# Kernel tuning notes

Hardware: AMD Instinct MI355X
Metric: run time of the kernel (lower is better)

The kernel has to match this reference:

```python
import jax, jax.numpy as jnp
import numpy as np

N, NB, EU, ED, EB = 40000, 60000, 200000, 200000, 120000
D, H = 256, 256
BN_EPS = 1e-5


def _bn(x, g, b):
    # training-mode BatchNorm1d over the cell dimension (biased variance)
    mu = jnp.mean(x, axis=0)
    var = jnp.mean((x - mu) ** 2, axis=0)
    return g * (x - mu) * jax.lax.rsqrt(var + BN_EPS) + b


def _mlp(x, W1, b1, g1, c1, W2, b2, g2, c2):
    # update nn: Linear -> BN -> ReLU -> Linear -> BN -> ReLU
    h = jax.nn.relu(_bn(x @ W1 + b1, g1, c1))
    return jax.nn.relu(_bn(h @ W2 + b2, g2, c2))


def _forward(x, up_attr, down_attr, boundary_attr, Wmu, bmu, Wmd, bmd,
             W1u, b1u, g1u, c1u, W2u, b2u, g2u, c2u,
             W1d, b1d, g1d, c1d, W2d, b2d, g2d, c2d,
             W1b, b1b, g1b, c1b, W2b, b2b, g2b, c2b,
             Wc, bc, gc, cc, eps1, eps2, eps3,
             up_index, down_index, boundary_index):
    n, d = x.shape
    # msg_up_nn = ReLU(Linear(cat[x_j, up_attr])); split W to avoid materializing cat
    mu = jax.nn.relu(x[up_index[0]] @ Wmu[:d] + up_attr @ Wmu[d:] + bmu)
    agg_up = jax.ops.segment_sum(mu, up_index[1], num_segments=n)
    md = jax.nn.relu(x[down_index[0]] @ Wmd[:d] + down_attr @ Wmd[d:] + bmd)
    agg_down = jax.ops.segment_sum(md, down_index[1], num_segments=n)
    # msg_boundaries_nn is identity: gather boundary cell features, sum to targets
    agg_bnd = jax.ops.segment_sum(boundary_attr[boundary_index[0]], boundary_index[1], num_segments=n)
    out_up = _mlp(agg_up + (1.0 + eps1) * x, W1u, b1u, g1u, c1u, W2u, b2u, g2u, c2u)
    out_down = _mlp(agg_down + (1.0 + eps2) * x, W1d, b1d, g1d, c1d, W2d, b2d, g2d, c2d)
    out_bnd = _mlp(agg_bnd + (1.0 + eps3) * x, W1b, b1b, g1b, c1b, W2b, b2b, g2b, c2b)
    comb = jnp.concatenate([out_up, out_down, out_bnd], axis=-1)
    return jax.nn.relu(_bn(comb @ Wc + bc, gc, cc))


def setup_inputs() -> dict:
    key = jax.random.key(0)
    ks = iter(jax.random.split(key, 64))

    def nrm(shape, scale=1.0):
        return jax.random.normal(next(ks), shape, dtype=jnp.float32) * scale

    inp = {}
    inp['x'] = nrm((N, D))
    inp['up_attr'] = nrm((EU, D))
    inp['down_attr'] = nrm((ED, D))
    inp['boundary_attr'] = nrm((NB, D))
    s_msg = 1.0 / np.sqrt(2 * D)
    inp['Wmu'] = nrm((2 * D, D), s_msg); inp['bmu'] = jnp.zeros((D,), jnp.float32)
    inp['Wmd'] = nrm((2 * D, D), s_msg); inp['bmd'] = jnp.zeros((D,), jnp.float32)
    s1, s2 = 1.0 / np.sqrt(D), 1.0 / np.sqrt(H)
    for t in ('u', 'd', 'b'):
        inp['W1' + t] = nrm((D, H), s1); inp['b1' + t] = jnp.zeros((H,), jnp.float32)
        inp['g1' + t] = jnp.ones((H,), jnp.float32); inp['c1' + t] = jnp.zeros((H,), jnp.float32)
        inp['W2' + t] = nrm((H, H), s2); inp['b2' + t] = jnp.zeros((H,), jnp.float32)
        inp['g2' + t] = jnp.ones((H,), jnp.float32); inp['c2' + t] = jnp.zeros((H,), jnp.float32)
    inp['Wc'] = nrm((3 * H, H), 1.0 / np.sqrt(3 * H)); inp['bc'] = jnp.zeros((H,), jnp.float32)
    inp['gc'] = jnp.ones((H,), jnp.float32); inp['cc'] = jnp.zeros((H,), jnp.float32)
    inp['eps1'] = jnp.zeros((1,), jnp.float32)
    inp['eps2'] = jnp.zeros((1,), jnp.float32)
    inp['eps3'] = jnp.zeros((1,), jnp.float32)
    inp['up_index'] = jax.random.randint(next(ks), (2, EU), 0, N)
    inp['down_index'] = jax.random.randint(next(ks), (2, ED), 0, N)
    bsrc = jax.random.randint(next(ks), (EB,), 0, NB)
    btgt = jax.random.randint(next(ks), (EB,), 0, N)
    inp['boundary_index'] = jnp.stack([bsrc, btgt], axis=0)
    return inp


def reference(x, up_attr, down_attr, boundary_attr, Wmu, bmu, Wmd, bmd,
              W1u, b1u, g1u, c1u, W2u, b2u, g2u, c2u,
              W1d, b1d, g1d, c1d, W2d, b2d, g2d, c2d,
              W1b, b1b, g1b, c1b, W2b, b2b, g2b, c2b,
              Wc, bc, gc, cc, eps1, eps2, eps3,
              up_index, down_index, boundary_index):
    return _forward(x, up_attr, down_attr, boundary_attr, Wmu, bmu, Wmd, bmd,
                    W1u, b1u, g1u, c1u, W2u, b2u, g2u, c2u,
                    W1d, b1d, g1d, c1d, W2d, b2d, g2d, c2d,
                    W1b, b1b, g1b, c1b, W2b, b2b, g2b, c2b,
                    Wc, bc, gc, cc, eps1, eps2, eps3,
                    up_index, down_index, boundary_index)
```

## Files before the change

kernel.cpp:

```cpp
#include <hip/hip_runtime.h>
#include <hip/hip_bf16.h>
#include <stdint.h>

#define NCELL 40000
#define EUE   200000
#define EDE   200000
#define EBE   120000
#define NM    ((size_t)NCELL * 256)

typedef __attribute__((ext_vector_type(8))) short bf16x8;
typedef __attribute__((ext_vector_type(4))) float f32x4;

__device__ __forceinline__ uint16_t f2bf(float f) {
  union { float f; uint32_t u; } v; v.f = f;
  uint32_t u = v.u;
  u += 0x7fffu + ((u >> 16) & 1u);
  return (uint16_t)(u >> 16);
}

struct WArgs {
  const float* src[11];
  uint16_t*    dst[11];
  int          K[11];
};

__global__ void k_wconv(WArgs a) {
  int m = blockIdx.z;
  int K = a.K[m];
  int k0 = blockIdx.x * 32;
  if (k0 >= K) return;
  int n0 = blockIdx.y * 32;
  __shared__ float t[32][33];
  int tx = threadIdx.x, ty = threadIdx.y;
  const float* src = a.src[m];
  for (int i = ty; i < 32; i += 8)
    t[i][tx] = src[(size_t)(k0 + i) * 256 + n0 + tx];
  __syncthreads();
  uint16_t* dst = a.dst[m];
  for (int i = ty; i < 32; i += 8)
    dst[(size_t)(n0 + i) * K + k0 + tx] = f2bf(t[tx][i]);
}

__global__ void k_count(const int* __restrict__ tgt, int* __restrict__ cnt, int E) {
  int i = blockIdx.x * 256 + threadIdx.x;
  if (i < E) atomicAdd(&cnt[tgt[i]], 1);
}

struct ScanArgs { const int* cnt[3]; int* offs[3]; int* head[3]; };

__global__ void k_scan(ScanArgs a) {
  int s = blockIdx.x;
  const int n = NCELL;
  const int* cnt = a.cnt[s];
  int* offs = a.offs[s];
  int* head = a.head[s];
  __shared__ int buf[1024];
  __shared__ int carry;
  int tid = threadIdx.x;
  if (tid == 0) carry = 0;
  __syncthreads();
  for (int base = 0; base < n; base += 1024) {
    int i = base + tid;
    int v = (i < n) ? cnt[i] : 0;
    buf[tid] = v;
    __syncthreads();
    for (int d = 1; d < 1024; d <<= 1) {
      int t = (tid >= d) ? buf[tid - d] : 0;
      __syncthreads();
      buf[tid] += t;
      __syncthreads();
    }
    int excl = carry + buf[tid] - v;
    if (i < n) { offs[i] = excl; head[i] = excl; }
    __syncthreads();
    if (tid == 1023) carry += buf[1023];
    __syncthreads();
  }
  if (tid == 0) offs[n] = carry;
}

__global__ void k_fill(const int* __restrict__ src, const int* __restrict__ tgt,
                       int* __restrict__ head, int* __restrict__ perm,
                       int* __restrict__ psrc, int E) {
  int e = blockIdx.x * 256 + threadIdx.x;
  if (e < E) {
    int p = atomicAdd(&head[tgt[e]], 1);
    perm[p] = e;
    psrc[p] = src[e];
  }
}

__global__ void k_segsum(const float* __restrict__ MSG, const int* __restrict__ offs,
                         const float* __restrict__ x, const float* __restrict__ eps,
                         float* __restrict__ out) {
  int t = blockIdx.x;
  int c = threadIdx.x * 4;
  int s = offs[t], e = offs[t + 1];
  float sE = 1.f + *eps;
  float4 xa = *(const float4*)(x + (size_t)t * 256 + c);
  float a0 = xa.x * sE, a1 = xa.y * sE, a2 = xa.z * sE, a3 = xa.w * sE;
  for (int j = s; j < e; j++) {
    float4 v = *(const float4*)(MSG + (size_t)j * 256 + c);
    a0 += v.x; a1 += v.y; a2 += v.z; a3 += v.w;
  }
  *(float4*)(out + (size_t)t * 256 + c) = make_float4(a0, a1, a2, a3);
}

__global__ void k_bgather(const float* __restrict__ battr, const int* __restrict__ offs,
                          const int* __restrict__ psrc, const float* __restrict__ x,
                          const float* __restrict__ eps, float* __restrict__ out) {
  int t = blockIdx.x;
  int c = threadIdx.x * 4;
  int s = offs[t], e = offs[t + 1];
  float sE = 1.f + *eps;
  float4 xa = *(const float4*)(x + (size_t)t * 256 + c);
  float a0 = xa.x * sE, a1 = xa.y * sE, a2 = xa.z * sE, a3 = xa.w * sE;
  for (int j = s; j < e; j++) {
    int sr = psrc[j];
    float4 v = *(const float4*)(battr + (size_t)sr * 256 + c);
    a0 += v.x; a1 += v.y; a2 += v.z; a3 += v.w;
  }
  *(float4*)(out + (size_t)t * 256 + c) = make_float4(a0, a1, a2, a3);
}

__global__ void k_bnrelu(const float* __restrict__ Y, const float* __restrict__ s12,
                         const float* __restrict__ g, const float* __restrict__ cb,
                         float* __restrict__ out, int ldo) {
  int i = blockIdx.x * 256 + threadIdx.x;
  int c = (i & 63) * 4;
  size_t row = (size_t)(i >> 6);
  const float invN = 1.f / (float)NCELL;
  float4 v = *(const float4*)(Y + row * 256 + c);
  float vv[4] = {v.x, v.y, v.z, v.w};
  float o[4];
#pragma unroll
  for (int k = 0; k < 4; k++) {
    float mean = s12[c + k] * invN;
    float var  = s12[256 + c + k] * invN - mean * mean;
    float sc = g[c + k] * rsqrtf(var + 1e-5f);
    float sh = cb[c + k] - mean * sc;
    o[k] = fmaxf(vv[k] * sc + sh, 0.f);
  }
  *(float4*)(out + row * (size_t)ldo + c) = make_float4(o[0], o[1], o[2], o[3]);
}

template <int MODE>
__global__ __launch_bounds__(256)
void k_gemm(const float* __restrict__ A, int lda, const uint16_t* __restrict__ Bt, int K,
            const float* __restrict__ bias, float* __restrict__ C, float* __restrict__ stats,
            const int* __restrict__ perm, const int* __restrict__ psrc,
            const float* __restrict__ XT, int M) {
  __shared__ uint16_t Al[128 * 32];
  __shared__ uint16_t Bl[128 * 32];
  const int tid = threadIdx.x;
  const int m0 = blockIdx.x * 128;
  const int n0 = blockIdx.y * 128;
  const int lane = tid & 63;
  const int wave = tid >> 6;
  const int wr = (wave >> 1) * 64;
  const int wc = (wave & 1) * 64;
  const int lm = lane & 15;
  const int lq = lane >> 4;

  f32x4 acc[4][4];
#pragma unroll
  for (int i = 0; i < 4; i++)
#pragma unroll
    for (int j = 0; j < 4; j++)
      acc[i][j] = f32x4{0.f, 0.f, 0.f, 0.f};

  const int arow = tid >> 3;
  const int acol = (tid & 7) * 4;

  int pidx[4];
#pragma unroll
  for (int rr = 0; rr < 4; rr++) {
    int gr = m0 + arow + rr * 32;
    if (MODE == 1) pidx[rr] = (gr < M) ? perm[gr] : -1;
    else           pidx[rr] = (gr < M) ? gr : -1;
  }

  for (int kt = 0; kt < K; kt += 32) {
#pragma unroll
    for (int rr = 0; rr < 4; rr++) {
      int r = arow + rr * 32;
      float4 v = make_float4(0.f, 0.f, 0.f, 0.f);
      if (pidx[rr] >= 0) v = *(const float4*)(A + (size_t)pidx[rr] * lda + kt + acol);
      union { uint16_t h[4]; uint2 u; } p;
      p.h[0] = f2bf(v.x); p.h[1] = f2bf(v.y); p.h[2] = f2bf(v.z); p.h[3] = f2bf(v.w);
      *(uint2*)(Al + r * 32 + acol) = p.u;
    }
#pragma unroll
    for (int ss = 0; ss < 2; ss++) {
      int j = tid + ss * 256;
      int row = j >> 2, kp = (j & 3) * 8;
      uint4 bv = *(const uint4*)(Bt + (size_t)(n0 + row) * K + kt + kp);
      *(uint4*)(Bl + row * 32 + kp) = bv;
    }
    __syncthreads();
    bf16x8 af[4], bfr[4];
#pragma unroll
    for (int i = 0; i < 4; i++)
      af[i] = *(const bf16x8*)(Al + (wr + 16 * i + lm) * 32 + lq * 8);
#pragma unroll
    for (int j = 0; j < 4; j++)
      bfr[j] = *(const bf16x8*)(Bl + (wc + 16 * j + lm) * 32 + lq * 8);
#pragma unroll
    for (int i = 0; i < 4; i++)
#pragma unroll
      for (int j = 0; j < 4; j++)
        acc[i][j] = __builtin_amdgcn_mfma_f32_16x16x32_bf16(af[i], bfr[j], acc[i][j], 0, 0, 0);
    __syncthreads();
  }

  const int cb0 = n0 + wc + lm;
  float bj[4];
#pragma unroll
  for (int j = 0; j < 4; j++) bj[j] = bias ? bias[cb0 + 16 * j] : 0.f;

  if (MODE == 0) {
    float s1l[4] = {0.f, 0.f, 0.f, 0.f}, s2l[4] = {0.f, 0.f, 0.f, 0.f};
#pragma unroll
    for (int i = 0; i < 4; i++) {
      int rbase = m0 + wr + 16 * i + lq * 4;
#pragma unroll
      for (int r = 0; r < 4; r++) {
        int row = rbase + r;
        if (row < M) {
#pragma unroll
          for (int j = 0; j < 4; j++) {
            float v = acc[i][j][r] + bj[j];
            C[(size_t)row * 256 + cb0 + 16 * j] = v;
            s1l[j] += v;
            s2l[j] += v * v;
          }
        }
      }
    }
    if (stats) {
      float* sb0 = (float*)Al;
      float* sb1 = sb0 + 128;
      __syncthreads();
      sb0[tid < 256 ? tid : 0] = 0.f;
      __syncthreads();
#pragma unroll
      for (int j = 0; j < 4; j++) {
        int colloc = wc + lm + 16 * j;
        atomicAdd(&sb0[colloc], s1l[j]);
        atomicAdd(&sb1[colloc], s2l[j]);
      }
      __syncthreads();
      if (tid < 128) {
        atomicAdd(&stats[n0 + tid],       sb0[tid]);
        atomicAdd(&stats[256 + n0 + tid], sb1[tid]);
      }
    }
  } else {
#pragma unroll
    for (int i = 0; i < 4; i++) {
      int rbase = m0 + wr + 16 * i + lq * 4;
#pragma unroll
      for (int r = 0; r < 4; r++) {
        int row = rbase + r;
        if (row < M) {
          int sr = psrc[row];
          const float* xr = XT + (size_t)sr * 256;
#pragma unroll
          for (int j = 0; j < 4; j++) {
            float v = acc[i][j][r] + xr[cb0 + 16 * j] + bj[j];
            C[(size_t)row * 256 + cb0 + 16 * j] = fmaxf(v, 0.f);
          }
        }
      }
    }
  }
}

extern "C" void kernel_launch(void* const* d_in, const int* in_sizes, int n_in,
                              void* d_out, int out_size, void* d_ws, size_t ws_size,
                              hipStream_t stream) {
  const float* x    = (const float*)d_in[0];
  const float* upA  = (const float*)d_in[1];
  const float* dnA  = (const float*)d_in[2];
  const float* bA   = (const float*)d_in[3];
  const float* Wmu  = (const float*)d_in[4];
  const float* bmu  = (const float*)d_in[5];
  const float* Wmd  = (const float*)d_in[6];
  const float* bmd  = (const float*)d_in[7];
  const float* W1[3] = {(const float*)d_in[8],  (const float*)d_in[16], (const float*)d_in[24]};
  const float* b1[3] = {(const float*)d_in[9],  (const float*)d_in[17], (const float*)d_in[25]};
  const float* g1[3] = {(const float*)d_in[10], (const float*)d_in[18], (const float*)d_in[26]};
  const float* c1[3] = {(const float*)d_in[11], (const float*)d_in[19], (const float*)d_in[27]};
  const float* W2[3] = {(const float*)d_in[12], (const float*)d_in[20], (const float*)d_in[28]};
  const float* b2[3] = {(const float*)d_in[13], (const float*)d_in[21], (const float*)d_in[29]};
  const float* g2[3] = {(const float*)d_in[14], (const float*)d_in[22], (const float*)d_in[30]};
  const float* c2[3] = {(const float*)d_in[15], (const float*)d_in[23], (const float*)d_in[31]};
  const float* Wc   = (const float*)d_in[32];
  const float* bc   = (const float*)d_in[33];
  const float* gc   = (const float*)d_in[34];
  const float* cc   = (const float*)d_in[35];
  const float* e1   = (const float*)d_in[36];
  const float* e2   = (const float*)d_in[37];
  const float* e3   = (const float*)d_in[38];
  const int* upI = (const int*)d_in[39];
  const int* dnI = (const int*)d_in[40];
  const int* bI  = (const int*)d_in[41];

  float* base = (float*)d_ws;
  size_t o = 0;
  float* XU   = base + o; o += NM;
  float* XD   = base + o; o += NM;
  float* ACC0 = base + o; o += NM;
  float* ACC1 = base + o; o += NM;
  float* ACC2 = base + o; o += NM;
  float* POOL = base + o; o += (size_t)200000 * 256;
  float* CAT  = POOL;
  float* Y    = POOL + (size_t)NCELL * 768;
  float* Z    = Y + NM;
  float* MSG  = POOL;
  float* STATS = base + o; o += 7 * 512;
  uint16_t* wb = (uint16_t*)(base + o); o += 600000;
  uint16_t* WmuAt = wb;
  uint16_t* WmuBt = wb + 1 * 65536;
  uint16_t* WmdAt = wb + 2 * 65536;
  uint16_t* WmdBt = wb + 3 * 65536;
  uint16_t* W1t[3] = {wb + 4 * 65536, wb + 5 * 65536, wb + 6 * 65536};
  uint16_t* W2t[3] = {wb + 7 * 65536, wb + 8 * 65536, wb + 9 * 65536};
  uint16_t* Wct    = wb + 10 * 65536;
  int* ib = (int*)(base + o);
  int* offsU = ib;
  int* offsD = ib + 40001;
  int* offsB = ib + 80002;
  int* headU = ib + 120003;
  int* headD = ib + 160003;
  int* headB = ib + 200003;
  int* permU = ib + 240003;
  int* psrcU = ib + 440003;
  int* permD = ib + 640003;
  int* psrcD = ib + 840003;
  int* permB = ib + 1040003;
  int* psrcB = ib + 1160003;

  float* ACCs[3] = {ACC0, ACC1, ACC2};

  hipMemsetAsync(STATS, 0, 7 * 512 * sizeof(float), stream);
  hipMemsetAsync(headU, 0, 3 * 40000 * sizeof(int), stream);

  WArgs wa;
  wa.src[0] = Wmu;               wa.dst[0] = WmuAt;  wa.K[0] = 256;
  wa.src[1] = Wmu + 256 * 256;   wa.dst[1] = WmuBt;  wa.K[1] = 256;
  wa.src[2] = Wmd;               wa.dst[2] = WmdAt;  wa.K[2] = 256;
  wa.src[3] = Wmd + 256 * 256;   wa.dst[3] = WmdBt;  wa.K[3] = 256;
  for (int t = 0; t < 3; t++) {
    wa.src[4 + 2 * t] = W1[t];   wa.dst[4 + 2 * t] = W1t[t]; wa.K[4 + 2 * t] = 256;
    wa.src[5 + 2 * t] = W2[t];   wa.dst[5 + 2 * t] = W2t[t]; wa.K[5 + 2 * t] = 256;
  }
  wa.src[10] = Wc; wa.dst[10] = Wct; wa.K[10] = 768;
  k_wconv<<<dim3(24, 8, 11), dim3(32, 8), 0, stream>>>(wa);

  k_count<<<(EUE + 255) / 256, 256, 0, stream>>>(upI + EUE, headU, EUE);
  k_count<<<(EDE + 255) / 256, 256, 0, stream>>>(dnI + EDE, headD, EDE);
  k_count<<<(EBE + 255) / 256, 256, 0, stream>>>(bI + EBE, headB, EBE);
  ScanArgs sa;
  sa.cnt[0] = headU; sa.offs[0] = offsU; sa.head[0] = headU;
  sa.cnt[1] = headD; sa.offs[1] = offsD; sa.head[1] = headD;
  sa.cnt[2] = headB; sa.offs[2] = offsB; sa.head[2] = headB;
  k_scan<<<3, 1024, 0, stream>>>(sa);
  k_fill<<<(EUE + 255) / 256, 256, 0, stream>>>(upI, upI + EUE, headU, permU, psrcU, EUE);
  k_fill<<<(EDE + 255) / 256, 256, 0, stream>>>(dnI, dnI + EDE, headD, permD, psrcD, EDE);
  k_fill<<<(EBE + 255) / 256, 256, 0, stream>>>(bI, bI + EBE, headB, permB, psrcB, EBE);

  const dim3 gN((NCELL + 127) / 128, 2);
  const dim3 gE((EUE + 127) / 128, 2);

  k_gemm<0><<<gN, 256, 0, stream>>>(x, 256, WmuAt, 256, nullptr, XU, nullptr,
                                    nullptr, nullptr, nullptr, NCELL);
  k_gemm<0><<<gN, 256, 0, stream>>>(x, 256, WmdAt, 256, nullptr, XD, nullptr,
                                    nullptr, nullptr, nullptr, NCELL);

  k_gemm<1><<<gE, 256, 0, stream>>>(upA, 256, WmuBt, 256, bmu, MSG, nullptr,
                                    permU, psrcU, XU, EUE);
  k_segsum<<<NCELL, 64, 0, stream>>>(MSG, offsU, x, e1, ACC0);

  k_gemm<1><<<gE, 256, 0, stream>>>(dnA, 256, WmdBt, 256, bmd, MSG, nullptr,
                                    permD, psrcD, XD, EDE);
  k_segsum<<<NCELL, 64, 0, stream>>>(MSG, offsD, x, e2, ACC1);

  k_bgather<<<NCELL, 64, 0, stream>>>(bA, offsB, psrcB, x, e3, ACC2);

  for (int t = 0; t < 3; t++) {
    float* S1 = STATS + 512 * (2 * t);
    float* S2 = STATS + 512 * (2 * t + 1);
    k_gemm<0><<<gN, 256, 0, stream>>>(ACCs[t], 256, W1t[t], 256, b1[t], Y, S1,
                                      nullptr, nullptr, nullptr, NCELL);
    k_bnrelu<<<10000, 256, 0, stream>>>(Y, S1, g1[t], c1[t], Z, 256);
    k_gemm<0><<<gN, 256, 0, stream>>>(Z, 256, W2t[t], 256, b2[t], Y, S2,
                                      nullptr, nullptr, nullptr, NCELL);
    k_bnrelu<<<10000, 256, 0, stream>>>(Y, S2, g2[t], c2[t], CAT + 256 * t, 768);
  }

  float* SC = STATS + 512 * 6;
  k_gemm<0><<<gN, 256, 0, stream>>>(CAT, 768, Wct, 768, bc, Y, SC,
                                    nullptr, nullptr, nullptr, NCELL);
  k_bnrelu<<<10000, 256, 0, stream>>>(Y, SC, gc, cc, (float*)d_out, 256);
}
```

Measured before the change: 1.618 ms.

## Fuse BatchNorm-ReLU into following GEMM loads and gather messages via permutation

Applies the BN scale/shift and ReLU while loading A tiles in the second MLP GEMM and the combine GEMM, removing most standalone bnrelu passes and the concat buffer. The edge message GEMM now reads edge attributes in original order (coalesced), and the segment sum gathers message rows through the permutation instead. It also adds a grouped block-index swizzle for the GEMMs and packs four cells per segsum/gather block with a 2-way unrolled loop. The cost is recomputing BN coefficients per tile and making the segment-sum reads random.

```diff
diff --git a/kernel.cpp b/kernel.cpp
--- a/kernel.cpp
+++ b/kernel.cpp
@@ -91,17 +91,25 @@
 }
 
 __global__ void k_segsum(const float* __restrict__ MSG, const int* __restrict__ offs,
-                         const float* __restrict__ x, const float* __restrict__ eps,
-                         float* __restrict__ out) {
-  int t = blockIdx.x;
+                         const int* __restrict__ perm, const float* __restrict__ x,
+                         const float* __restrict__ eps, float* __restrict__ out) {
+  int t = blockIdx.x * 4 + threadIdx.y;
   int c = threadIdx.x * 4;
   int s = offs[t], e = offs[t + 1];
   float sE = 1.f + *eps;
   float4 xa = *(const float4*)(x + (size_t)t * 256 + c);
   float a0 = xa.x * sE, a1 = xa.y * sE, a2 = xa.z * sE, a3 = xa.w * sE;
-  for (int j = s; j < e; j++) {
-    float4 v = *(const float4*)(MSG + (size_t)j * 256 + c);
-    a0 += v.x; a1 += v.y; a2 += v.z; a3 += v.w;
+  int j = s;
+  for (; j + 1 < e; j += 2) {
+    int r0 = perm[j], r1 = perm[j + 1];
+    float4 v0 = *(const float4*)(MSG + (size_t)r0 * 256 + c);
+    float4 v1 = *(const float4*)(MSG + (size_t)r1 * 256 + c);
+    a0 += v0.x + v1.x; a1 += v0.y + v1.y; a2 += v0.z + v1.z; a3 += v0.w + v1.w;
+  }
+  if (j < e) {
+    int r0 = perm[j];
+    float4 v0 = *(const float4*)(MSG + (size_t)r0 * 256 + c);
+    a0 += v0.x; a1 += v0.y; a2 += v0.z; a3 += v0.w;
   }
   *(float4*)(out + (size_t)t * 256 + c) = make_float4(a0, a1, a2, a3);
 }
@@ -109,16 +117,23 @@
 __global__ void k_bgather(const float* __restrict__ battr, const int* __restrict__ offs,
                           const int* __restrict__ psrc, const float* __restrict__ x,
                           const float* __restrict__ eps, float* __restrict__ out) {
-  int t = blockIdx.x;
+  int t = blockIdx.x * 4 + threadIdx.y;
   int c = threadIdx.x * 4;
   int s = offs[t], e = offs[t + 1];
   float sE = 1.f + *eps;
   float4 xa = *(const float4*)(x + (size_t)t * 256 + c);
   float a0 = xa.x * sE, a1 = xa.y * sE, a2 = xa.z * sE, a3 = xa.w * sE;
-  for (int j = s; j < e; j++) {
-    int sr = psrc[j];
-    float4 v = *(const float4*)(battr + (size_t)sr * 256 + c);
-    a0 += v.x; a1 += v.y; a2 += v.z; a3 += v.w;
+  int j = s;
+  for (; j + 1 < e; j += 2) {
+    int r0 = psrc[j], r1 = psrc[j + 1];
+    float4 v0 = *(const float4*)(battr + (size_t)r0 * 256 + c);
+    float4 v1 = *(const float4*)(battr + (size_t)r1 * 256 + c);
+    a0 += v0.x + v1.x; a1 += v0.y + v1.y; a2 += v0.z + v1.z; a3 += v0.w + v1.w;
+  }
+  if (j < e) {
+    int r0 = psrc[j];
+    float4 v0 = *(const float4*)(battr + (size_t)r0 * 256 + c);
+    a0 += v0.x; a1 += v0.y; a2 += v0.z; a3 += v0.w;
   }
   *(float4*)(out + (size_t)t * 256 + c) = make_float4(a0, a1, a2, a3);
 }
@@ -144,17 +159,36 @@
   *(float4*)(out + row * (size_t)ldo + c) = make_float4(o[0], o[1], o[2], o[3]);
 }
 
-template <int MODE>
+struct CCArgs { const float* g[3]; const float* c[3]; float* Gg; float* Gc; };
+__global__ void k_concat(CCArgs a) {
+  int t = blockIdx.x, i = threadIdx.x;
+  a.Gg[t * 256 + i] = a.g[t][i];
+  a.Gc[t * 256 + i] = a.c[t][i];
+}
+
+template <int MODE, int FUSEBN>
 __global__ __launch_bounds__(256)
-void k_gemm(const float* __restrict__ A, int lda, const uint16_t* __restrict__ Bt, int K,
-            const float* __restrict__ bias, float* __restrict__ C, float* __restrict__ stats,
-            const int* __restrict__ perm, const int* __restrict__ psrc,
-            const float* __restrict__ XT, int M) {
+void k_gemm(const float* __restrict__ A, const uint16_t* __restrict__ Bt, int K,
+            const float* __restrict__ bias, float* __restrict__ C,
+            float* __restrict__ stats, float* __restrict__ statsq,
+            const float* __restrict__ bnS, const float* __restrict__ bnG,
+            const float* __restrict__ bnC, const int* __restrict__ srcIdx,
+            const float* __restrict__ XT, int M, int gx) {
   __shared__ uint16_t Al[128 * 32];
   __shared__ uint16_t Bl[128 * 32];
   const int tid = threadIdx.x;
-  const int m0 = blockIdx.x * 128;
-  const int n0 = blockIdx.y * 128;
+  int id = blockIdx.x;
+  int body2 = (gx & ~7) * 2;
+  int m0, n0;
+  if (id < body2) {
+    int g = id >> 4, j = id & 15;
+    m0 = ((g << 3) + (j & 7)) * 128;
+    n0 = (j >> 3) * 128;
+  } else {
+    int r = id - body2, rem = gx & 7;
+    m0 = ((gx & ~7) + (r % rem)) * 128;
+    n0 = (r / rem) * 128;
+  }
   const int lane = tid & 63;
   const int wave = tid >> 6;
   const int wr = (wave >> 1) * 64;
@@ -176,16 +210,42 @@
 #pragma unroll
   for (int rr = 0; rr < 4; rr++) {
     int gr = m0 + arow + rr * 32;
-    if (MODE == 1) pidx[rr] = (gr < M) ? perm[gr] : -1;
-    else           pidx[rr] = (gr < M) ? gr : -1;
-  }
-
+    pidx[rr] = (gr < M) ? gr : -1;
+  }
+
+  const float invN = 1.f / (float)NCELL;
   for (int kt = 0; kt < K; kt += 32) {
+    float sc[4], sh[4];
+    if (FUSEBN) {
+#pragma unroll
+      for (int k2 = 0; k2 < 4; k2++) {
+        int col = kt + acol + k2;
+        float mean = bnS[col] * invN;
+        float var  = bnS[K + col] * invN - mean * mean;
+        float s = bnG[col] * rsqrtf(var + 1e-5f);
+        sc[k2] = s; sh[k2] = bnC[col] - mean * s;
+      }
+    }
 #pragma unroll
     for (int rr = 0; rr < 4; rr++) {
       int r = arow + rr * 32;
       float4 v = make_float4(0.f, 0.f, 0.f, 0.f);
-      if (pidx[rr] >= 0) v = *(const float4*)(A + (size_t)pidx[rr] * lda + kt + acol);
+      if (pidx[rr] >= 0) {
+        const float* ap;
+        if (MODE == 2) {
+          int ct = kt + acol;
+          ap = A + (size_t)(ct >> 8) * NM + (size_t)pidx[rr] * 256 + (ct & 255);
+        } else {
+          ap = A + (size_t)pidx[rr] * 256 + kt + acol;
+        }
+        v = *(const float4*)ap;
+      }
+      if (FUSEBN) {
+        v.x = fmaxf(v.x * sc[0] + sh[0], 0.f);
+        v.y = fmaxf(v.y * sc[1] + sh[1], 0.f);
+        v.z = fmaxf(v.z * sc[2] + sh[2], 0.f);
+        v.w = fmaxf(v.w * sc[3] + sh[3], 0.f);
+      }
       union { uint16_t h[4]; uint2 u; } p;
       p.h[0] = f2bf(v.x); p.h[1] = f2bf(v.y); p.h[2] = f2bf(v.z); p.h[3] = f2bf(v.w);
       *(uint2*)(Al + r * 32 + acol) = p.u;
@@ -218,7 +278,25 @@
 #pragma unroll
   for (int j = 0; j < 4; j++) bj[j] = bias ? bias[cb0 + 16 * j] : 0.f;
 
-  if (MODE == 0) {
+  if (MODE == 1) {
+#pragma unroll
+    for (int i = 0; i < 4; i++) {
+      int rbase = m0 + wr + 16 * i + lq * 4;
+#pragma unroll
+      for (int r = 0; r < 4; r++) {
+        int row = rbase + r;
+        if (row < M) {
+          int sr = srcIdx[row];
+          const float* xr = XT + (size_t)sr * 256;
+#pragma unroll
+          for (int j = 0; j < 4; j++) {
+            float v = acc[i][j][r] + xr[cb0 + 16 * j] + bj[j];
+            C[(size_t)row * 256 + cb0 + 16 * j] = fmaxf(v, 0.f);
+          }
+        }
+      }
+    }
+  } else {
     float s1l[4] = {0.f, 0.f, 0.f, 0.f}, s2l[4] = {0.f, 0.f, 0.f, 0.f};
 #pragma unroll
     for (int i = 0; i < 4; i++) {
@@ -241,7 +319,7 @@
       float* sb0 = (float*)Al;
       float* sb1 = sb0 + 128;
       __syncthreads();
-      sb0[tid < 256 ? tid : 0] = 0.f;
+      sb0[tid] = 0.f;
       __syncthreads();
 #pragma unroll
       for (int j = 0; j < 4; j++) {
@@ -251,26 +329,8 @@
       }
       __syncthreads();
       if (tid < 128) {
-        atomicAdd(&stats[n0 + tid],       sb0[tid]);
-        atomicAdd(&stats[256 + n0 + tid], sb1[tid]);
-      }
-    }
-  } else {
-#pragma unroll
-    for (int i = 0; i < 4; i++) {
-      int rbase = m0 + wr + 16 * i + lq * 4;
-#pragma unroll
-      for (int r = 0; r < 4; r++) {
-        int row = rbase + r;
-        if (row < M) {
-          int sr = psrc[row];
-          const float* xr = XT + (size_t)sr * 256;
-#pragma unroll
-          for (int j = 0; j < 4; j++) {
-            float v = acc[i][j][r] + xr[cb0 + 16 * j] + bj[j];
-            C[(size_t)row * 256 + cb0 + 16 * j] = fmaxf(v, 0.f);
-          }
-        }
+        atomicAdd(&stats[n0 + tid],  sb0[tid]);
+        atomicAdd(&statsq[n0 + tid], sb1[tid]);
       }
     }
   }
@@ -313,12 +373,16 @@
   float* ACC0 = base + o; o += NM;
   float* ACC1 = base + o; o += NM;
   float* ACC2 = base + o; o += NM;
-  float* POOL = base + o; o += (size_t)200000 * 256;
-  float* CAT  = POOL;
-  float* Y    = POOL + (size_t)NCELL * 768;
-  float* Z    = Y + NM;
+  float* POOL = base + o; o += 5 * NM;
   float* MSG  = POOL;
-  float* STATS = base + o; o += 7 * 512;
+  float* Y3   = POOL;
+  float* Y1   = POOL + 3 * NM;
+  float* Yf   = POOL + 4 * NM;
+  float* STATS = base + o; o += 3584;
+  float* SCAT = STATS + 1536;
+  float* SC   = STATS + 3072;
+  float* GCg  = base + o; o += 768;
+  float* GCc  = base + o; o += 768;
   uint16_t* wb = (uint16_t*)(base + o); o += 600000;
   uint16_t* WmuAt = wb;
   uint16_t* WmuBt = wb + 1 * 65536;
@@ -343,7 +407,7 @@
 
   float* ACCs[3] = {ACC0, ACC1, ACC2};
 
-  hipMemsetAsync(STATS, 0, 7 * 512 * sizeof(float), stream);
+  hipMemsetAsync(STATS, 0, 3584 * sizeof(float), stream);
   hipMemsetAsync(headU, 0, 3 * 40000 * sizeof(int), stream);
 
   WArgs wa;
@@ -357,6 +421,11 @@
   }
   wa.src[10] = Wc; wa.dst[10] = Wct; wa.K[10] = 768;
   k_wconv<<<dim3(24, 8, 11), dim3(32, 8), 0, stream>>>(wa);
+
+  CCArgs ca;
+  for (int t = 0; t < 3; t++) { ca.g[t] = g2[t]; ca.c[t] = c2[t]; }
+  ca.Gg = GCg; ca.Gc = GCc;
+  k_concat<<<3, 256, 0, stream>>>(ca);
 
   k_count<<<(EUE + 255) / 256, 256, 0, stream>>>(upI + EUE, headU, EUE);
   k_count<<<(EDE + 255) / 256, 256, 0, stream>>>(dnI + EDE, headD, EDE);
@@ -370,37 +439,33 @@
   k_fill<<<(EDE + 255) / 256, 256, 0, stream>>>(dnI, dnI + EDE, headD, permD, psrcD, EDE);
   k_fill<<<(EBE + 255) / 256, 256, 0, stream>>>(bI, bI + EBE, headB, permB, psrcB, EBE);
 
-  const dim3 gN((NCELL + 127) / 128, 2);
-  const dim3 gE((EUE + 127) / 128, 2);
-
-  k_gemm<0><<<gN, 256, 0, stream>>>(x, 256, WmuAt, 256, nullptr, XU, nullptr,
-                                    nullptr, nullptr, nullptr, NCELL);
-  k_gemm<0><<<gN, 256, 0, stream>>>(x, 256, WmdAt, 256, nullptr, XD, nullptr,
-                                    nullptr, nullptr, nullptr, NCELL);
-
-  k_gemm<1><<<gE, 256, 0, stream>>>(upA, 256, WmuBt, 256, bmu, MSG, nullptr,
-                                    permU, psrcU, XU, EUE);
-  k_segsum<<<NCELL, 64, 0, stream>>>(MSG, offsU, x, e1, ACC0);
-
-  k_gemm<1><<<gE, 256, 0, stream>>>(dnA, 256, WmdBt, 256, bmd, MSG, nullptr,
-                                    permD, psrcD, XD, EDE);
-  k_segsum<<<NCELL, 64, 0, stream>>>(MSG, offsD, x, e2, ACC1);
-
-  k_bgather<<<NCELL, 64, 0, stream>>>(bA, offsB, psrcB, x, e3, ACC2);
+  const int gxN = (NCELL + 127) / 128;
+  const int gxE = (EUE + 127) / 128;
+
+  k_gemm<0, 0><<<gxN * 2, 256, 0, stream>>>(x, WmuAt, 256, nullptr, XU,
+      nullptr, nullptr, nullptr, nullptr, nullptr, nullptr, nullptr, NCELL, gxN);
+  k_gemm<0, 0><<<gxN * 2, 256, 0, stream>>>(x, WmdAt, 256, nullptr, XD,
+      nullptr, nullptr, nullptr, nullptr, nullptr, nullptr, nullptr, NCELL, gxN);
+
+  k_gemm<1, 0><<<gxE * 2, 256, 0, stream>>>(upA, WmuBt, 256, bmu, MSG,
+      nullptr, nullptr, nullptr, nullptr, nullptr, upI, XU, EUE, gxE);
+  k_segsum<<<10000, dim3(64, 4), 0, stream>>>(MSG, offsU, permU, x, e1, ACC0);
+
+  k_gemm<1, 0><<<gxE * 2, 256, 0, stream>>>(dnA, WmdBt, 256, bmd, MSG,
+      nullptr, nullptr, nullptr, nullptr, nullptr, dnI, XD, EDE, gxE);
+  k_segsum<<<10000, dim3(64, 4), 0, stream>>>(MSG, offsD, permD, x, e2, ACC1);
+
+  k_bgather<<<10000, dim3(64, 4), 0, stream>>>(bA, offsB, psrcB, x, e3, ACC2);
 
   for (int t = 0; t < 3; t++) {
-    float* S1 = STATS + 512 * (2 * t);
-    float* S2 = STATS + 512 * (2 * t + 1);
-    k_gemm<0><<<gN, 256, 0, stream>>>(ACCs[t], 256, W1t[t], 256, b1[t], Y, S1,
-                                      nullptr, nullptr, nullptr, NCELL);
-    k_bnrelu<<<10000, 256, 0, stream>>>(Y, S1, g1[t], c1[t], Z, 256);
-    k_gemm<0><<<gN, 256, 0, stream>>>(Z, 256, W2t[t], 256, b2[t], Y, S2,
-                                      nullptr, nullptr, nullptr, NCELL);
-    k_bnrelu<<<10000, 256, 0, stream>>>(Y, S2, g2[t], c2[t], CAT + 256 * t, 768);
-  }
-
-  float* SC = STATS + 512 * 6;
-  k_gemm<0><<<gN, 256, 0, stream>>>(CAT, 768, Wct, 768, bc, Y, SC,
-                                    nullptr, nullptr, nullptr, NCELL);
-  k_bnrelu<<<10000, 256, 0, stream>>>(Y, SC, gc, cc, (float*)d_out, 256);
-}
+    float* S1 = STATS + 512 * t;
+    k_gemm<0, 0><<<gxN * 2, 256, 0, stream>>>(ACCs[t], W1t[t], 256, b1[t], Y1,
+        S1, S1 + 256, nullptr, nullptr, nullptr, nullptr, nullptr, NCELL, gxN);
+    k_gemm<0, 1><<<gxN * 2, 256, 0, stream>>>(Y1, W2t[t], 256, b2[t], Y3 + t * NM,
+        SCAT + t * 256, SCAT + 768 + t * 256, S1, g1[t], c1[t], nullptr, nullptr, NCELL, gxN);
+  }
+
+  k_gemm<2, 1><<<gxN * 2, 256, 0, stream>>>(Y3, Wct, 768, bc, Yf,
+      SC, SC + 256, SCAT, GCg, GCc, nullptr, nullptr, NCELL, gxN);
+  k_bnrelu<<<10000, 256, 0, stream>>>(Yf, SC, gc, cc, (float*)d_out, 256);
+}
```

Result: faster. 1.489 ms (-8.0%).
